# Optimization experiments

Measured on AMD Instinct MI355X. Metric: run time of the kernel, lower is better.

The kernel has to match this reference:

```python
import jax, jax.numpy as jnp
import numpy as np
from jax import lax

B, S, T = 256, 128, 64
IN, MID, HID = 4, 128, 512
NH = 4  # attention heads


def setup_inputs() -> dict:
    key = jax.random.key(0)
    ks = iter(jax.random.split(key, 64))
    def p(*shape):
        return jax.random.normal(next(ks), shape, jnp.float32) * 0.05
    d = {}
    d["src"] = jax.random.normal(next(ks), (B, S, IN), jnp.float32)
    d["trg"] = jax.random.normal(next(ks), (B, T, IN), jnp.float32)
    # fc_in: IN -> MID//4 -> MID//2 -> MID
    d["fi_w1"] = p(MID // 4, IN); d["fi_b1"] = p(MID // 4)
    d["fi_w2"] = p(MID // 2, MID // 4); d["fi_b2"] = p(MID // 2)
    d["fi_w3"] = p(MID, MID // 2); d["fi_b3"] = p(MID)
    # encoder: 2-layer bidirectional LSTM (layer0 in=MID, layer1 in=2*HID)
    for name, ind in [("e0", MID), ("e1", 2 * HID)]:
        for sfx in ["f", "b"]:
            d[name + sfx + "_wih"] = p(4 * HID, ind)
            d[name + sfx + "_whh"] = p(4 * HID, HID)
            d[name + sfx + "_bih"] = p(4 * HID)
            d[name + sfx + "_bhh"] = p(4 * HID)
    d["attnfc_w"] = p(MID, 2 * HID); d["attnfc_b"] = p(MID)
    d["inproj_w"] = p(3 * MID, MID); d["inproj_b"] = p(3 * MID)
    d["outproj_w"] = p(MID, MID); d["outproj_b"] = p(MID)
    # decoder: 2-layer unidirectional LSTM (layer0 in=MID, layer1 in=HID)
    for name, ind in [("d0", MID), ("d1", HID)]:
        d[name + "_wih"] = p(4 * HID, ind)
        d[name + "_whh"] = p(4 * HID, HID)
        d[name + "_bih"] = p(4 * HID)
        d[name + "_bhh"] = p(4 * HID)
    # fc_out: HID -> MID//2 -> MID//4 -> IN
    d["fo_w1"] = p(MID // 2, HID); d["fo_b1"] = p(MID // 2)
    d["fo_w2"] = p(MID // 4, MID // 2); d["fo_b2"] = p(MID // 4)
    d["fo_w3"] = p(IN, MID // 4); d["fo_b3"] = p(IN)
    return d


def _gelu(x):
    return jax.nn.gelu(x, approximate=False)  # torch default GELU is exact


def _mlp3(x, w1, b1, w2, b2, w3, b3):
    h = _gelu(x @ w1.T + b1)
    h = _gelu(h @ w2.T + b2)
    return h @ w3.T + b3


def _lstm(x, h0, c0, wih, whh, bih, bhh, reverse=False):
    """PyTorch-semantics LSTM layer. x: (B,T,in) -> (hs (B,T,H), h_T, c_T)."""
    xg = jnp.einsum('bti,gi->btg', x, wih) + (bih + bhh)  # fold input GEMM over time
    def step(carry, xt):
        h, c = carry
        g = xt + h @ whh.T
        i, f, gg, o = jnp.split(g, 4, axis=-1)  # torch gate order: i,f,g,o
        c = jax.nn.sigmoid(f) * c + jax.nn.sigmoid(i) * jnp.tanh(gg)
        h = jax.nn.sigmoid(o) * jnp.tanh(c)
        return (h, c), h
    (h, c), hs = lax.scan(step, (h0, c0), jnp.swapaxes(xg, 0, 1), reverse=reverse)
    return jnp.swapaxes(hs, 0, 1), h, c


def _mha(q_in, kv, inproj_w, inproj_b, outproj_w, outproj_b):
    E = q_in.shape[-1]
    dh = E // NH
    wq, wk, wv = jnp.split(inproj_w, 3, axis=0)
    bq, bk, bv = jnp.split(inproj_b, 3)
    q = q_in @ wq.T + bq
    k = kv @ wk.T + bk
    v = kv @ wv.T + bv
    hd = lambda x: x.reshape(x.shape[0], x.shape[1], NH, dh)
    scores = jnp.einsum('bqhd,bkhd->bhqk', hd(q), hd(k)) * (1.0 / float(np.sqrt(dh)))
    a = jax.nn.softmax(scores, axis=-1)
    o = jnp.einsum('bhqk,bkhd->bqhd', a, hd(v)).reshape(q.shape)
    return o @ outproj_w.T + outproj_b


def reference(src, trg,
              fi_w1, fi_b1, fi_w2, fi_b2, fi_w3, fi_b3,
              e0f_wih, e0f_whh, e0f_bih, e0f_bhh, e0b_wih, e0b_whh, e0b_bih, e0b_bhh,
              e1f_wih, e1f_whh, e1f_bih, e1f_bhh, e1b_wih, e1b_whh, e1b_bih, e1b_bhh,
              attnfc_w, attnfc_b, inproj_w, inproj_b, outproj_w, outproj_b,
              d0_wih, d0_whh, d0_bih, d0_bhh, d1_wih, d1_whh, d1_bih, d1_bhh,
              fo_w1, fo_b1, fo_w2, fo_b2, fo_w3, fo_b3):
    bsz = src.shape[0]
    z = jnp.zeros((bsz, HID), src.dtype)
    enc_embed = _mlp3(src, fi_w1, fi_b1, fi_w2, fi_b2, fi_w3, fi_b3)
    # encoder layer 0 (bidirectional)
    l0f, hf0, cf0 = _lstm(enc_embed, z, z, e0f_wih, e0f_whh, e0f_bih, e0f_bhh)
    l0b, hb0, cb0 = _lstm(enc_embed, z, z, e0b_wih, e0b_whh, e0b_bih, e0b_bhh, reverse=True)
    x1 = jnp.concatenate([l0f, l0b], axis=-1)
    # encoder layer 1 (bidirectional)
    l1f, hf1, cf1 = _lstm(x1, z, z, e1f_wih, e1f_whh, e1f_bih, e1f_bhh)
    l1b, hb1, cb1 = _lstm(x1, z, z, e1b_wih, e1b_whh, e1b_bih, e1b_bhh, reverse=True)
    enc_out = jnp.concatenate([l1f, l1b], axis=-1)  # (B,S,2H)
    # h.view(L,2,B,H).sum(dim=1): sum forward+backward final states per layer
    h_l0, c_l0 = hf0 + hb0, cf0 + cb0
    h_l1, c_l1 = hf1 + hb1, cf1 + cb1
    proj_enc = jnp.tanh(enc_out @ attnfc_w.T + attnfc_b)  # (B,S,MID)
    # teacher_forcing_ratio = 1.0 -> decoder inputs are exactly trg[:, 0:T]
    inp = _mlp3(trg, fi_w1, fi_b1, fi_w2, fi_b2, fi_w3, fi_b3)  # (B,T,MID)
    attn_out = _mha(inp, proj_enc, inproj_w, inproj_b, outproj_w, outproj_b)
    dec_input = inp + attn_out
    d0, _, _ = _lstm(dec_input, h_l0, c_l0, d0_wih, d0_whh, d0_bih, d0_bhh)
    d1, _, _ = _lstm(d0, h_l1, c_l1, d1_wih, d1_whh, d1_bih, d1_bhh)
    delta = _mlp3(d1, fo_w1, fo_b1, fo_w2, fo_b2, fo_w3, fo_b3)
    return trg + delta  # pred_t = trg[:, t-1] + delta_t
```

## Files before the change

### kernel.cpp

```cpp
#include <hip/hip_runtime.h>
#include <cstdint>
#include <cstddef>
#include <cstdio>

typedef __bf16 bf16;
typedef __bf16 bf16x8 __attribute__((ext_vector_type(8)));
typedef __bf16 bf16x4 __attribute__((ext_vector_type(4)));
typedef float f32x4 __attribute__((ext_vector_type(4)));

#define DEVFN __device__ __forceinline__

DEVFN float geluf(float x) { return 0.5f * x * (1.0f + erff(x * 0.70710678118654752f)); }
DEVFN float sigmoidf(float x) { return 1.0f / (1.0f + expf(-x)); }

template <int WGM, int WGN, int ACT, bool RES>
__launch_bounds__(WGM * WGN * 64)
__global__ void gemm_bt(const bf16* __restrict__ A, const bf16* __restrict__ W,
                        const float* __restrict__ bias, const bf16* __restrict__ Rsd,
                        bf16* __restrict__ C, int M, int N, int K) {
  constexpr int BM = WGM * 64, BN = WGN * 64, T = WGM * WGN * 64;
  constexpr int NA = BM * 4 / T, NB = BN * 4 / T;
  __shared__ __align__(16) char ldsA[BM * 64];
  __shared__ __align__(16) char ldsB[BN * 64];
  const int tid = threadIdx.x;
  const int lane = tid & 63, wave = tid >> 6;
  const int wm = wave % WGM, wn = wave / WGM;
  const int l16 = lane & 15, quad = lane >> 4;
  const int bm0 = blockIdx.x * BM, bn0 = blockIdx.y * BN;

  f32x4 acc[4][4] = {};
  for (int k0 = 0; k0 < K; k0 += 32) {
    bf16x8 ta[NA], tb[NB];
#pragma unroll
    for (int i = 0; i < NA; ++i) {
      int lin = i * T + tid;
      int row = lin >> 2, seg = lin & 3;
      ta[i] = *(const bf16x8*)(A + (size_t)(bm0 + row) * K + k0 + seg * 8);
    }
#pragma unroll
    for (int i = 0; i < NB; ++i) {
      int lin = i * T + tid;
      int row = lin >> 2, seg = lin & 3;
      tb[i] = *(const bf16x8*)(W + (size_t)(bn0 + row) * K + k0 + seg * 8);
    }
#pragma unroll
    for (int i = 0; i < NA; ++i) *(bf16x8*)(ldsA + (i * T + tid) * 16) = ta[i];
#pragma unroll
    for (int i = 0; i < NB; ++i) *(bf16x8*)(ldsB + (i * T + tid) * 16) = tb[i];
    __syncthreads();
    bf16x8 af[4], bfrag[4];
#pragma unroll
    for (int mi = 0; mi < 4; ++mi)
      af[mi] = *(const bf16x8*)(ldsA + (wm * 64 + mi * 16 + l16) * 64 + quad * 16);
#pragma unroll
    for (int ni = 0; ni < 4; ++ni)
      bfrag[ni] = *(const bf16x8*)(ldsB + (wn * 64 + ni * 16 + l16) * 64 + quad * 16);
#pragma unroll
    for (int mi = 0; mi < 4; ++mi)
#pragma unroll
      for (int ni = 0; ni < 4; ++ni)
        acc[mi][ni] = __builtin_amdgcn_mfma_f32_16x16x32_bf16(af[mi], bfrag[ni], acc[mi][ni], 0, 0, 0);
    __syncthreads();
  }
#pragma unroll
  for (int mi = 0; mi < 4; ++mi) {
#pragma unroll
    for (int ni = 0; ni < 4; ++ni) {
      int col = bn0 + wn * 64 + ni * 16 + l16;
      float bv = bias[col];
#pragma unroll
      for (int r = 0; r < 4; ++r) {
        int row = bm0 + wm * 64 + mi * 16 + quad * 4 + r;
        float x = acc[mi][ni][r] + bv;
        if (ACT == 1) x = tanhf(x);
        if (ACT == 2) x = geluf(x);
        size_t idx = (size_t)row * N + col;
        if (RES) x += (float)Rsd[idx];
        C[idx] = (bf16)x;
      }
    }
  }
}

template <int WGM, int WGN, int ACT>
__launch_bounds__(WGM * WGN * 64)
__global__ void gemm_hcA(const bf16* __restrict__ HC, int tbase, const bf16* __restrict__ W,
                         const float* __restrict__ bias, bf16* __restrict__ C,
                         int M, int N, int K) {
  constexpr int BM = WGM * 64, BN = WGN * 64, T = WGM * WGN * 64;
  constexpr int NA = BM * 4 / T, NB = BN * 4 / T;
  __shared__ __align__(16) char ldsA[BM * 64];
  __shared__ __align__(16) char ldsB[BN * 64];
  const int tid = threadIdx.x;
  const int lane = tid & 63, wave = tid >> 6;
  const int wm = wave % WGM, wn = wave / WGM;
  const int l16 = lane & 15, quad = lane >> 4;
  const int bm0 = blockIdx.x * BM, bn0 = blockIdx.y * BN;

  f32x4 acc[4][4] = {};
  for (int k0 = 0; k0 < K; k0 += 32) {
    bf16x8 ta[NA], tb[NB];
#pragma unroll
    for (int i = 0; i < NA; ++i) {
      int lin = i * T + tid;
      int row = bm0 + (lin >> 2), seg = lin & 3;
      int t = tbase + (row >> 8), b = row & 255;
      ta[i] = *(const bf16x8*)(HC + (size_t)t * 262144 + (size_t)((k0 >> 3) + seg) * 2048 + b * 8);
    }
#pragma unroll
    for (int i = 0; i < NB; ++i) {
      int lin = i * T + tid;
      int row = lin >> 2, seg = lin & 3;
      tb[i] = *(const bf16x8*)(W + (size_t)(bn0 + row) * K + k0 + seg * 8);
    }
#pragma unroll
    for (int i = 0; i < NA; ++i) *(bf16x8*)(ldsA + (i * T + tid) * 16) = ta[i];
#pragma unroll
    for (int i = 0; i < NB; ++i) *(bf16x8*)(ldsB + (i * T + tid) * 16) = tb[i];
    __syncthreads();
    bf16x8 af[4], bfrag[4];
#pragma unroll
    for (int mi = 0; mi < 4; ++mi)
      af[mi] = *(const bf16x8*)(ldsA + (wm * 64 + mi * 16 + l16) * 64 + quad * 16);
#pragma unroll
    for (int ni = 0; ni < 4; ++ni)
      bfrag[ni] = *(const bf16x8*)(ldsB + (wn * 64 + ni * 16 + l16) * 64 + quad * 16);
#pragma unroll
    for (int mi = 0; mi < 4; ++mi)
#pragma unroll
      for (int ni = 0; ni < 4; ++ni)
        acc[mi][ni] = __builtin_amdgcn_mfma_f32_16x16x32_bf16(af[mi], bfrag[ni], acc[mi][ni], 0, 0, 0);
    __syncthreads();
  }
#pragma unroll
  for (int mi = 0; mi < 4; ++mi) {
#pragma unroll
    for (int ni = 0; ni < 4; ++ni) {
      int col = bn0 + wn * 64 + ni * 16 + l16;
      float bv = bias[col];
#pragma unroll
      for (int r = 0; r < 4; ++r) {
        int row = bm0 + wm * 64 + mi * 16 + quad * 4 + r;
        float x = acc[mi][ni][r] + bv;
        if (ACT == 1) x = tanhf(x);
        if (ACT == 2) x = geluf(x);
        C[(size_t)row * N + col] = (bf16)x;
      }
    }
  }
}

__launch_bounds__(128)
__global__ void gemm_hc_fcout(const bf16* __restrict__ HC, const bf16* __restrict__ W,
                              const float* __restrict__ bias, bf16* __restrict__ C,
                              int M, int N, int K) {
  constexpr int WGM = 2, WGN = 1;
  constexpr int BM = WGM * 64, BN = WGN * 64, T = WGM * WGN * 64;
  constexpr int NA = BM * 4 / T, NB = BN * 4 / T;
  __shared__ __align__(16) char ldsA[BM * 64];
  __shared__ __align__(16) char ldsB[BN * 64];
  const int tid = threadIdx.x;
  const int lane = tid & 63, wave = tid >> 6;
  const int wm = wave % WGM, wn = wave / WGM;
  const int l16 = lane & 15, quad = lane >> 4;
  const int bm0 = blockIdx.x * BM, bn0 = blockIdx.y * BN;

  f32x4 acc[4][4] = {};
  for (int k0 = 0; k0 < K; k0 += 32) {
    bf16x8 ta[NA], tb[NB];
#pragma unroll
    for (int i = 0; i < NA; ++i) {
      int lin = i * T + tid;
      int row = bm0 + (lin >> 2), seg = lin & 3;
      int t = row >> 8, b = row & 255;
      ta[i] = *(const bf16x8*)(HC + (size_t)t * 131072 + (size_t)((k0 >> 3) + seg) * 2048 + b * 8);
    }
#pragma unroll
    for (int i = 0; i < NB; ++i) {
      int lin = i * T + tid;
      int row = lin >> 2, seg = lin & 3;
      tb[i] = *(const bf16x8*)(W + (size_t)(bn0 + row) * K + k0 + seg * 8);
    }
#pragma unroll
    for (int i = 0; i < NA; ++i) *(bf16x8*)(ldsA + (i * T + tid) * 16) = ta[i];
#pragma unroll
    for (int i = 0; i < NB; ++i) *(bf16x8*)(ldsB + (i * T + tid) * 16) = tb[i];
    __syncthreads();
    bf16x8 af[4], bfrag[4];
#pragma unroll
    for (int mi = 0; mi < 4; ++mi)
      af[mi] = *(const bf16x8*)(ldsA + (wm * 64 + mi * 16 + l16) * 64 + quad * 16);
#pragma unroll
    for (int ni = 0; ni < 4; ++ni)
      bfrag[ni] = *(const bf16x8*)(ldsB + (wn * 64 + ni * 16 + l16) * 64 + quad * 16);
#pragma unroll
    for (int mi = 0; mi < 4; ++mi)
#pragma unroll
      for (int ni = 0; ni < 4; ++ni)
        acc[mi][ni] = __builtin_amdgcn_mfma_f32_16x16x32_bf16(af[mi], bfrag[ni], acc[mi][ni], 0, 0, 0);
    __syncthreads();
  }
#pragma unroll
  for (int mi = 0; mi < 4; ++mi) {
#pragma unroll
    for (int ni = 0; ni < 4; ++ni) {
      int col = bn0 + wn * 64 + ni * 16 + l16;
      float bv = bias[col];
#pragma unroll
      for (int r = 0; r < 4; ++r) {
        int row = bm0 + wm * 64 + mi * 16 + quad * 4 + r;
        float x = geluf(acc[mi][ni][r] + bv);
        C[(size_t)row * N + col] = (bf16)x;
      }
    }
  }
}

template <int HCMODE>
DEVFN void xg_tile(const bf16* __restrict__ A, int tbase, const bf16* __restrict__ W,
                   const float* __restrict__ bias, bf16* __restrict__ C,
                   int K, int bm0, int bn0, int tid, bf16* ldsA, bf16* ldsB) {
  const int lane = tid & 63, wave = tid >> 6;
  const int wm = wave & 1, wn = wave >> 1;
  const int l16 = lane & 15, quad = lane >> 4;
  f32x4 acc[4][4] = {};
  for (int k0 = 0; k0 < K; k0 += 32) {
    bf16x8 ta, tb0, tb1;
    {
      int row = bm0 + (tid >> 2), seg = tid & 3;
      if (HCMODE) {
        int t = tbase + (row >> 8), b = row & 255;
        ta = *(const bf16x8*)(A + (size_t)t * 262144 + (size_t)((k0 >> 3) + seg) * 2048 + b * 8);
      } else {
        ta = *(const bf16x8*)(A + (size_t)row * K + k0 + seg * 8);
      }
    }
    { int row = tid >> 2, seg = tid & 3;
      tb0 = *(const bf16x8*)(W + (size_t)(bn0 + row) * K + k0 + seg * 8); }
    { int lin = 512 + tid; int row = lin >> 2, seg = lin & 3;
      tb1 = *(const bf16x8*)(W + (size_t)(bn0 + row) * K + k0 + seg * 8); }
    *(bf16x8*)(ldsA + tid * 8) = ta;
    *(bf16x8*)(ldsB + tid * 8) = tb0;
    *(bf16x8*)(ldsB + (512 + tid) * 8) = tb1;
    __syncthreads();
    bf16x8 af[4], bfr[4];
#pragma unroll
    for (int mi = 0; mi < 4; ++mi)
      af[mi] = *(const bf16x8*)(ldsA + (wm * 64 + mi * 16 + l16) * 32 + quad * 8);
#pragma unroll
    for (int ni = 0; ni < 4; ++ni)
      bfr[ni] = *(const bf16x8*)(ldsB + (wn * 64 + ni * 16 + l16) * 32 + quad * 8);
#pragma unroll
    for (int mi = 0; mi < 4; ++mi)
#pragma unroll
      for (int ni = 0; ni < 4; ++ni)
        acc[mi][ni] = __builtin_amdgcn_mfma_f32_16x16x32_bf16(af[mi], bfr[ni], acc[mi][ni], 0, 0, 0);
    __syncthreads();
  }
#pragma unroll
  for (int mi = 0; mi < 4; ++mi) {
#pragma unroll
    for (int ni = 0; ni < 4; ++ni) {
      int col = bn0 + wn * 64 + ni * 16 + l16;
      float bv = bias[col];
#pragma unroll
      for (int r = 0; r < 4; ++r) {
        int row = bm0 + wm * 64 + mi * 16 + quad * 4 + r;
        C[(size_t)row * 2048 + col] = (bf16)(acc[mi][ni][r] + bv);
      }
    }
  }
}

struct RDir {
  const bf16* whh_r;
  const bf16* xg;
  bf16* hc;
  int slcOff, rev;
  const bf16* h0;
  float* cbuf;
  bf16* hfin;
};

struct GJob {
  int mode;
  const bf16* Af; const bf16* Ab;
  int tbF, tbB;
  const bf16* Wf; const bf16* Wb;
  const float* bsF; const float* bsB;
  bf16* outF; bf16* outB;
};

__launch_bounds__(512, 1)
__global__ void lstm_rec_g(RDir da, RDir db, int t0, int tc, int Tfull,
                           int* __restrict__ cnts, GJob job) {
  __shared__ __align__(16) char smem[36864];
  const int blk = blockIdx.x;
  const int tid = threadIdx.x;

  if (blk >= 128) {
    if (job.mode == 0) return;
    bf16* ldsA = (bf16*)smem;
    bf16* ldsB = (bf16*)(smem + 8192);
    const int gb = blk - 128;
    const int K = (job.mode == 2) ? 1024 : 128;
    for (int tile = gb; tile < 512; tile += 128) {
      int dir = tile >> 8;
      int rem = tile & 255;
      int mi = rem >> 3, ni = rem & 7;
      const bf16* A = dir ? job.Ab : job.Af;
      int tb = dir ? job.tbB : job.tbF;
      const bf16* W = dir ? job.Wb : job.Wf;
      const float* bs = dir ? job.bsB : job.bsF;
      bf16* C = dir ? job.outB : job.outF;
      if (job.mode == 2)
        xg_tile<1>(A, tb, W, bs, C, K, mi * 128, ni * 256, tid, ldsA, ldsB);
      else
        xg_tile<0>(A, tb, W, bs, C, K, mi * 128, ni * 256, tid, ldsA, ldsB);
    }
    return;
  }

  bf16* whh_lds = (bf16*)smem;
  bf16* hstg = (bf16*)(smem + 32768);
  const RDir d = (blk >= 64) ? db : da;
  const int slice = blk & 63;
  const int colBase = slice * 32, unitBase = slice * 8;
  const int w = tid >> 6, lane = tid & 63;
  const int l16 = lane & 15, quad = lane >> 4;

  for (int e = tid * 8; e < 32 * 512; e += 512 * 8) {
    int c = e >> 9, k0 = e & 511;
    bf16x8 v = *(const bf16x8*)(d.whh_r + (size_t)(colBase + c) * 512 + k0);
    *(bf16x8*)(whh_lds + ((k0 >> 3) << 8) + (c << 3)) = v;
  }
  float cst[2][2];
#pragma unroll
  for (int m = 0; m < 2; ++m)
#pragma unroll
    for (int i = 0; i < 2; ++i) {
      int b = (w * 2 + i) * 16 + l16;
      cst[m][i] = d.cbuf[(size_t)b * 512 + unitBase + m * 4 + quad];
    }
  __syncthreads();

  int* cnt = cnts + (blk & 64);
  const int b0 = (w * 2) * 16 + l16;
  const int b1 = b0 + 16;

  for (int s = 0; s < tc; ++s) {
    const int sg = t0 + s;
    const int t = d.rev ? (Tfull - 1 - sg) : sg;
    const int lt = d.rev ? (tc - 1 - s) : s;

    bf16x4 gxr[2][2];
#pragma unroll
    for (int m = 0; m < 2; ++m)
#pragma unroll
      for (int i = 0; i < 2; ++i) {
        int b = b0 + i * 16;
        gxr[m][i] = *(const bf16x4*)(d.xg + ((size_t)lt * 256 + b) * 2048 + colBase + m * 16 + quad * 4);
      }
    bf16x8 hr[16][2];
    if (sg == 0) {
      const bf16* hp0 = d.h0 + (size_t)b0 * 512 + quad * 8;
      const bf16* hp1 = d.h0 + (size_t)b1 * 512 + quad * 8;
#pragma unroll
      for (int kk = 0; kk < 16; ++kk) {
        hr[kk][0] = *(const bf16x8*)(hp0 + kk * 32);
        hr[kk][1] = *(const bf16x8*)(hp1 + kk * 32);
      }
    } else {
      const int tp = d.rev ? (t + 1) : (t - 1);
      const bf16* hc = d.hc + (size_t)tp * 262144 + (size_t)d.slcOff * 2048;
#pragma unroll
      for (int kk = 0; kk < 16; ++kk) {
        int u8 = kk * 4 + quad;
        hr[kk][0] = *(const bf16x8*)(hc + u8 * 2048 + (size_t)b0 * 8);
        hr[kk][1] = *(const bf16x8*)(hc + u8 * 2048 + (size_t)b1 * 8);
      }
    }
    __builtin_amdgcn_sched_barrier(0);

    f32x4 acc[2][2] = {};
#pragma unroll
    for (int kk = 0; kk < 16; ++kk) {
      bf16x8 a0 = *(const bf16x8*)(whh_lds + kk * 1024 + quad * 256 + l16 * 8);
      bf16x8 a1 = *(const bf16x8*)(whh_lds + kk * 1024 + quad * 256 + 128 + l16 * 8);
      acc[0][0] = __builtin_amdgcn_mfma_f32_16x16x32_bf16(a0, hr[kk][0], acc[0][0], 0, 0, 0);
      acc[1][0] = __builtin_amdgcn_mfma_f32_16x16x32_bf16(a1, hr[kk][0], acc[1][0], 0, 0, 0);
      acc[0][1] = __builtin_amdgcn_mfma_f32_16x16x32_bf16(a0, hr[kk][1], acc[0][1], 0, 0, 0);
      acc[1][1] = __builtin_amdgcn_mfma_f32_16x16x32_bf16(a1, hr[kk][1], acc[1][1], 0, 0, 0);
    }
#pragma unroll
    for (int m = 0; m < 2; ++m)
#pragma unroll
      for (int i = 0; i < 2; ++i) {
        float gi = acc[m][i][0] + (float)gxr[m][i][0];
        float gf = acc[m][i][1] + (float)gxr[m][i][1];
        float gg = acc[m][i][2] + (float)gxr[m][i][2];
        float go = acc[m][i][3] + (float)gxr[m][i][3];
        float cn = sigmoidf(gf) * cst[m][i] + sigmoidf(gi) * tanhf(gg);
        float hv = sigmoidf(go) * tanhf(cn);
        cst[m][i] = cn;
        int b = (w * 2 + i) * 16 + l16;
        hstg[b * 8 + m * 4 + quad] = (bf16)hv;
      }
    __syncthreads();
    {
      unsigned long long v = *(const unsigned long long*)(hstg + tid * 4);
      __hip_atomic_store((unsigned long long*)(d.hc + (size_t)t * 262144 +
                                               (size_t)(d.slcOff + slice) * 2048 + tid * 4),
                         v, __ATOMIC_RELAXED, __HIP_MEMORY_SCOPE_AGENT);
    }
    __syncthreads();
    if (s < tc - 1 && tid == 0)
      __hip_atomic_fetch_add(cnt, 1, __ATOMIC_RELAXED, __HIP_MEMORY_SCOPE_AGENT);
    if (sg == Tfull - 1 && d.hfin && tid < 256) {
      const unsigned long long* p = (const unsigned long long*)(hstg + tid * 8);
      unsigned long long* r2 = (unsigned long long*)(d.hfin + (size_t)tid * 512 + unitBase);
      r2[0] = p[0]; r2[1] = p[1];
    }
    if (s < tc - 1) {
      if (w == 0) {
        int target = 64 * (s + 1), guard = 0;
        while (__hip_atomic_load(cnt, __ATOMIC_RELAXED, __HIP_MEMORY_SCOPE_AGENT) < target) {
          __builtin_amdgcn_s_sleep(2);
          if (++guard > (1 << 22)) break;
        }
      }
      __syncthreads();
    }
  }
#pragma unroll
  for (int m = 0; m < 2; ++m)
#pragma unroll
    for (int i = 0; i < 2; ++i) {
      int b = (w * 2 + i) * 16 + l16;
      d.cbuf[(size_t)b * 512 + unitBase + m * 4 + quad] = cst[m][i];
    }
}

__launch_bounds__(512, 1)
__global__ void lstm_dec_fused(
    const bf16* __restrict__ whh0, const bf16* __restrict__ xg0,
    bf16* __restrict__ hc0, const bf16* __restrict__ h0d0, float* __restrict__ c0buf,
    const bf16* __restrict__ whh1, const bf16* __restrict__ wih1, const float* __restrict__ bias1,
    bf16* __restrict__ hc1, const bf16* __restrict__ h0d1,
    float* __restrict__ c1buf, int* __restrict__ cnts) {
  const int blk = blockIdx.x;
  const int tid = threadIdx.x;
  const int w = tid >> 6, lane = tid & 63;
  const int l16 = lane & 15, quad = lane >> 4;
  constexpr int TC = 64;

  __shared__ __align__(16) bf16 wldsA[32 * 512];
  __shared__ __align__(16) bf16 wldsB[32 * 512];
  __shared__ __align__(16) bf16 hstg[256 * 8];

  int* cnt0 = cnts;
  int* cnt1 = cnts + 64;
  const int b0 = (w * 2) * 16 + l16;
  const int b1 = b0 + 16;

  if (blk < 64) {
    const int slice = blk;
    const int colBase = slice * 32;
    for (int e = tid * 8; e < 32 * 512; e += 512 * 8) {
      int c = e >> 9, k0 = e & 511;
      bf16x8 v = *(const bf16x8*)(whh0 + (size_t)(colBase + c) * 512 + k0);
      *(bf16x8*)(wldsA + ((k0 >> 3) << 8) + (c << 3)) = v;
    }
    float cst[2][2];
#pragma unroll
    for (int m = 0; m < 2; ++m)
#pragma unroll
      for (int i = 0; i < 2; ++i) {
        int b = (w * 2 + i) * 16 + l16;
        cst[m][i] = c0buf[(size_t)b * 512 + slice * 8 + m * 4 + quad];
      }
    __syncthreads();

    for (int s = 0; s < TC; ++s) {
      bf16x4 gxr[2][2];
#pragma unroll
      for (int m = 0; m < 2; ++m)
#pragma unroll
        for (int i = 0; i < 2; ++i) {
          int b = b0 + i * 16;
          gxr[m][i] = *(const bf16x4*)(xg0 + ((size_t)s * 256 + b) * 2048 + colBase + m * 16 + quad * 4);
        }
      bf16x8 hr[16][2];
      if (s == 0) {
        const bf16* hp0 = h0d0 + (size_t)b0 * 512 + quad * 8;
        const bf16* hp1 = h0d0 + (size_t)b1 * 512 + quad * 8;
#pragma unroll
        for (int kk = 0; kk < 16; ++kk) {
          hr[kk][0] = *(const bf16x8*)(hp0 + kk * 32);
          hr[kk][1] = *(const bf16x8*)(hp1 + kk * 32);
        }
      } else {
        const bf16* hc = hc0 + (size_t)(s - 1) * 131072;
#pragma unroll
        for (int kk = 0; kk < 16; ++kk) {
          int u8 = kk * 4 + quad;
          hr[kk][0] = *(const bf16x8*)(hc + u8 * 2048 + (size_t)b0 * 8);
          hr[kk][1] = *(const bf16x8*)(hc + u8 * 2048 + (size_t)b1 * 8);
        }
      }
      __builtin_amdgcn_sched_barrier(0);
      f32x4 acc[2][2] = {};
#pragma unroll
      for (int kk = 0; kk < 16; ++kk) {
        bf16x8 a0 = *(const bf16x8*)(wldsA + kk * 1024 + quad * 256 + l16 * 8);
        bf16x8 a1 = *(const bf16x8*)(wldsA + kk * 1024 + quad * 256 + 128 + l16 * 8);
        acc[0][0] = __builtin_amdgcn_mfma_f32_16x16x32_bf16(a0, hr[kk][0], acc[0][0], 0, 0, 0);
        acc[1][0] = __builtin_amdgcn_mfma_f32_16x16x32_bf16(a1, hr[kk][0], acc[1][0], 0, 0, 0);
        acc[0][1] = __builtin_amdgcn_mfma_f32_16x16x32_bf16(a0, hr[kk][1], acc[0][1], 0, 0, 0);
        acc[1][1] = __builtin_amdgcn_mfma_f32_16x16x32_bf16(a1, hr[kk][1], acc[1][1], 0, 0, 0);
      }
#pragma unroll
      for (int m = 0; m < 2; ++m)
#pragma unroll
        for (int i = 0; i < 2; ++i) {
          float gi = acc[m][i][0] + (float)gxr[m][i][0];
          float gf = acc[m][i][1] + (float)gxr[m][i][1];
          float gg = acc[m][i][2] + (float)gxr[m][i][2];
          float go = acc[m][i][3] + (float)gxr[m][i][3];
          float cn = sigmoidf(gf) * cst[m][i] + sigmoidf(gi) * tanhf(gg);
          float hv = sigmoidf(go) * tanhf(cn);
          cst[m][i] = cn;
          int b = (w * 2 + i) * 16 + l16;
          hstg[b * 8 + m * 4 + quad] = (bf16)hv;
        }
      __syncthreads();
      {
        unsigned long long v = *(const unsigned long long*)(hstg + tid * 4);
        __hip_atomic_store((unsigned long long*)(hc0 + (size_t)s * 131072 + slice * 2048 + tid * 4),
                           v, __ATOMIC_RELAXED, __HIP_MEMORY_SCOPE_AGENT);
      }
      __syncthreads();
      if (tid == 0)
        __hip_atomic_fetch_add(cnt0, 1, __ATOMIC_RELAXED, __HIP_MEMORY_SCOPE_AGENT);
      if (s < TC - 1) {
        if (w == 0) {
          int target = 64 * (s + 1), guard = 0;
          while (__hip_atomic_load(cnt0, __ATOMIC_RELAXED, __HIP_MEMORY_SCOPE_AGENT) < target) {
            __builtin_amdgcn_s_sleep(2);
            if (++guard > (1 << 22)) break;
          }
        }
        __syncthreads();
      }
    }
#pragma unroll
    for (int m = 0; m < 2; ++m)
#pragma unroll
      for (int i = 0; i < 2; ++i) {
        int b = (w * 2 + i) * 16 + l16;
        c0buf[(size_t)b * 512 + slice * 8 + m * 4 + quad] = cst[m][i];
      }
  } else {
    const int slice = blk - 64;
    const int colBase = slice * 32;
    for (int e = tid * 8; e < 32 * 512; e += 512 * 8) {
      int c = e >> 9, k0 = e & 511;
      bf16x8 v = *(const bf16x8*)(whh1 + (size_t)(colBase + c) * 512 + k0);
      *(bf16x8*)(wldsA + ((k0 >> 3) << 8) + (c << 3)) = v;
      bf16x8 u = *(const bf16x8*)(wih1 + (size_t)(colBase + c) * 512 + k0);
      *(bf16x8*)(wldsB + ((k0 >> 3) << 8) + (c << 3)) = u;
    }
    float gbv[2][4];
#pragma unroll
    for (int m = 0; m < 2; ++m)
#pragma unroll
      for (int r = 0; r < 4; ++r) gbv[m][r] = bias1[colBase + m * 16 + quad * 4 + r];
    float cst[2][2];
#pragma unroll
    for (int m = 0; m < 2; ++m)
#pragma unroll
      for (int i = 0; i < 2; ++i) {
        int b = (w * 2 + i) * 16 + l16;
        cst[m][i] = c1buf[(size_t)b * 512 + slice * 8 + m * 4 + quad];
      }
    __syncthreads();
    if (w == 0) {
      int guard = 0;
      while (__hip_atomic_load(cnt0, __ATOMIC_RELAXED, __HIP_MEMORY_SCOPE_AGENT) < 64) {
        __builtin_amdgcn_s_sleep(2);
        if (++guard > (1 << 22)) break;
      }
    }
    __syncthreads();

    for (int s = 0; s < TC; ++s) {
      f32x4 acc[2][2] = {};
      {
        const bf16* xc = hc0 + (size_t)s * 131072;
        bf16x8 xr[16][2];
#pragma unroll
        for (int kk = 0; kk < 16; ++kk) {
          int u8 = kk * 4 + quad;
          xr[kk][0] = *(const bf16x8*)(xc + u8 * 2048 + (size_t)b0 * 8);
          xr[kk][1] = *(const bf16x8*)(xc + u8 * 2048 + (size_t)b1 * 8);
        }
        __builtin_amdgcn_sched_barrier(0);
#pragma unroll
        for (int kk = 0; kk < 16; ++kk) {
          bf16x8 aw0 = *(const bf16x8*)(wldsB + kk * 1024 + quad * 256 + l16 * 8);
          bf16x8 aw1 = *(const bf16x8*)(wldsB + kk * 1024 + quad * 256 + 128 + l16 * 8);
          acc[0][0] = __builtin_amdgcn_mfma_f32_16x16x32_bf16(aw0, xr[kk][0], acc[0][0], 0, 0, 0);
          acc[1][0] = __builtin_amdgcn_mfma_f32_16x16x32_bf16(aw1, xr[kk][0], acc[1][0], 0, 0, 0);
          acc[0][1] = __builtin_amdgcn_mfma_f32_16x16x32_bf16(aw0, xr[kk][1], acc[0][1], 0, 0, 0);
          acc[1][1] = __builtin_amdgcn_mfma_f32_16x16x32_bf16(aw1, xr[kk][1], acc[1][1], 0, 0, 0);
        }
      }
      {
        bf16x8 hr[16][2];
        if (s == 0) {
          const bf16* hp0 = h0d1 + (size_t)b0 * 512 + quad * 8;
          const bf16* hp1 = h0d1 + (size_t)b1 * 512 + quad * 8;
#pragma unroll
          for (int kk = 0; kk < 16; ++kk) {
            hr[kk][0] = *(const bf16x8*)(hp0 + kk * 32);
            hr[kk][1] = *(const bf16x8*)(hp1 + kk * 32);
          }
        } else {
          const bf16* hc = hc1 + (size_t)(s - 1) * 131072;
#pragma unroll
          for (int kk = 0; kk < 16; ++kk) {
            int u8 = kk * 4 + quad;
            hr[kk][0] = *(const bf16x8*)(hc + u8 * 2048 + (size_t)b0 * 8);
            hr[kk][1] = *(const bf16x8*)(hc + u8 * 2048 + (size_t)b1 * 8);
          }
        }
        __builtin_amdgcn_sched_barrier(0);
#pragma unroll
        for (int kk = 0; kk < 16; ++kk) {
          bf16x8 a0 = *(const bf16x8*)(wldsA + kk * 1024 + quad * 256 + l16 * 8);
          bf16x8 a1 = *(const bf16x8*)(wldsA + kk * 1024 + quad * 256 + 128 + l16 * 8);
          acc[0][0] = __builtin_amdgcn_mfma_f32_16x16x32_bf16(a0, hr[kk][0], acc[0][0], 0, 0, 0);
          acc[1][0] = __builtin_amdgcn_mfma_f32_16x16x32_bf16(a1, hr[kk][0], acc[1][0], 0, 0, 0);
          acc[0][1] = __builtin_amdgcn_mfma_f32_16x16x32_bf16(a0, hr[kk][1], acc[0][1], 0, 0, 0);
          acc[1][1] = __builtin_amdgcn_mfma_f32_16x16x32_bf16(a1, hr[kk][1], acc[1][1], 0, 0, 0);
        }
      }
#pragma unroll
      for (int m = 0; m < 2; ++m)
#pragma unroll
        for (int i = 0; i < 2; ++i) {
          float gi = acc[m][i][0] + gbv[m][0];
          float gf = acc[m][i][1] + gbv[m][1];
          float gg = acc[m][i][2] + gbv[m][2];
          float go = acc[m][i][3] + gbv[m][3];
          float cn = sigmoidf(gf) * cst[m][i] + sigmoidf(gi) * tanhf(gg);
          float hv = sigmoidf(go) * tanhf(cn);
          cst[m][i] = cn;
          int b = (w * 2 + i) * 16 + l16;
          hstg[b * 8 + m * 4 + quad] = (bf16)hv;
        }
      __syncthreads();
      {
        unsigned long long v = *(const unsigned long long*)(hstg + tid * 4);
        __hip_atomic_store((unsigned long long*)(hc1 + (size_t)s * 131072 + slice * 2048 + tid * 4),
                           v, __ATOMIC_RELAXED, __HIP_MEMORY_SCOPE_AGENT);
      }
      __syncthreads();
      if (s < TC - 1) {
        if (tid == 0)
          __hip_atomic_fetch_add(cnt1, 1, __ATOMIC_RELAXED, __HIP_MEMORY_SCOPE_AGENT);
        if (w == 0) {
          int t1 = 64 * (s + 1), t0n = 64 * (s + 2), guard = 0;
          while (true) {
            int v1 = __hip_atomic_load(cnt1, __ATOMIC_RELAXED, __HIP_MEMORY_SCOPE_AGENT);
            int v0 = __hip_atomic_load(cnt0, __ATOMIC_RELAXED, __HIP_MEMORY_SCOPE_AGENT);
            if (v1 >= t1 && v0 >= t0n) break;
            __builtin_amdgcn_s_sleep(2);
            if (++guard > (1 << 22)) break;
          }
        }
        __syncthreads();
      }
    }
#pragma unroll
    for (int m = 0; m < 2; ++m)
#pragma unroll
      for (int i = 0; i < 2; ++i) {
        int b = (w * 2 + i) * 16 + l16;
        c1buf[(size_t)b * 512 + slice * 8 + m * 4 + quad] = cst[m][i];
      }
  }
}

__launch_bounds__(256)
__global__ void fc_in_mlp(const float* __restrict__ x, bf16* __restrict__ y, int rows, int tmod,
                          const float* __restrict__ w1, const float* __restrict__ b1,
                          const float* __restrict__ w2, const float* __restrict__ b2,
                          const float* __restrict__ w3, const float* __restrict__ b3) {
  __shared__ float sm[10592];
  const int tid = threadIdx.x;
  for (int i = tid; i < 10592; i += 256) {
    float v;
    if (i < 128) v = w1[i];
    else if (i < 160) v = b1[i - 128];
    else if (i < 2208) v = w2[i - 160];
    else if (i < 2272) v = b2[i - 2208];
    else if (i < 10464) v = w3[i - 2272];
    else v = b3[i - 10464];
    sm[i] = v;
  }
  __syncthreads();
  int row = blockIdx.x * 256 + tid;
  if (row >= rows) return;
  int orow = tmod ? ((row % tmod) * 256 + row / tmod) : row;
  float xin[4];
#pragma unroll
  for (int k = 0; k < 4; ++k) xin[k] = x[(size_t)row * 4 + k];
  float h1[32];
#pragma unroll
  for (int j = 0; j < 32; ++j) {
    float a = sm[128 + j];
#pragma unroll
    for (int k = 0; k < 4; ++k) a += sm[j * 4 + k] * xin[k];
    h1[j] = geluf(a);
  }
  float h2[64];
#pragma unroll
  for (int j = 0; j < 64; ++j) {
    float a = sm[2208 + j];
#pragma unroll
    for (int k = 0; k < 32; ++k) a += sm[160 + j * 32 + k] * h1[k];
    h2[j] = geluf(a);
  }
  for (int c = 0; c < 8; ++c) {
    float accv[16];
#pragma unroll
    for (int j = 0; j < 16; ++j) accv[j] = sm[10464 + c * 16 + j];
#pragma unroll
    for (int j = 0; j < 16; ++j) {
#pragma unroll
      for (int k = 0; k < 64; ++k) accv[j] += sm[2272 + (c * 16 + j) * 64 + k] * h2[k];
    }
#pragma unroll
    for (int j = 0; j < 16; ++j) y[(size_t)orow * 128 + c * 16 + j] = (bf16)accv[j];
  }
}

__launch_bounds__(256)
__global__ void fc_out_tail(const bf16* __restrict__ h1in, const float* __restrict__ trg,
                            float* __restrict__ out, int rows,
                            const float* __restrict__ w2, const float* __restrict__ b2,
                            const float* __restrict__ w3, const float* __restrict__ b3) {
  __shared__ float sm[2212];
  const int tid = threadIdx.x;
  for (int i = tid; i < 2212; i += 256) {
    float v;
    if (i < 2048) v = w2[i];
    else if (i < 2080) v = b2[i - 2048];
    else if (i < 2208) v = w3[i - 2080];
    else v = b3[i - 2208];
    sm[i] = v;
  }
  __syncthreads();
  int row = blockIdx.x * 256 + tid;
  if (row >= rows) return;
  int b = row >> 6, t = row & 63;
  const bf16* h1p = h1in + ((size_t)t * 256 + b) * 64;
  float h1[64];
#pragma unroll
  for (int k = 0; k < 64; ++k) h1[k] = (float)h1p[k];
  float h2[32];
#pragma unroll
  for (int j = 0; j < 32; ++j) {
    float a = sm[2048 + j];
#pragma unroll
    for (int k = 0; k < 64; ++k) a += sm[j * 64 + k] * h1[k];
    h2[j] = geluf(a);
  }
#pragma unroll
  for (int dd = 0; dd < 4; ++dd) {
    float a = sm[2208 + dd];
#pragma unroll
    for (int k = 0; k < 32; ++k) a += sm[2080 + dd * 32 + k] * h2[k];
    out[(size_t)row * 4 + dd] = trg[(size_t)row * 4 + dd] + a;
  }
}

__launch_bounds__(128)
__global__ void attention_kernel(const bf16* __restrict__ Q, const bf16* __restrict__ K,
                                 const bf16* __restrict__ V, bf16* __restrict__ O) {
  __shared__ bf16 qs[64 * 32];
  __shared__ float ks[128 * 33];
  __shared__ bf16 vs[128 * 32];
  __shared__ float sc[64 * 132];
  const int b = blockIdx.x, h = blockIdx.y, tid = threadIdx.x;
  for (int i = tid; i < 64 * 32; i += 128) {
    int t = i >> 5, dd = i & 31;
    qs[i] = Q[((size_t)t * 256 + b) * 128 + h * 32 + dd];
  }
  for (int i = tid; i < 128 * 32; i += 128) {
    int s = i >> 5, dd = i & 31;
    size_t ridx = ((size_t)s * 256 + b) * 128 + h * 32 + dd;
    ks[s * 33 + dd] = (float)K[ridx];
    vs[i] = V[ridx];
  }
  __syncthreads();
  const float scale = 0.17677669529663687f;
  for (int i = tid; i < 64 * 128; i += 128) {
    int t = i >> 7, s = i & 127;
    float a = 0.f;
#pragma unroll
    for (int dd = 0; dd < 32; ++dd) a += (float)qs[t * 32 + dd] * ks[s * 33 + dd];
    sc[t * 132 + s] = a * scale;
  }
  __syncthreads();
  if (tid < 64) {
    float m = -1e30f;
    for (int s = 0; s < 128; ++s) m = fmaxf(m, sc[tid * 132 + s]);
    float sum = 0.f;
    for (int s = 0; s < 128; ++s) { float e = expf(sc[tid * 132 + s] - m); sc[tid * 132 + s] = e; sum += e; }
    float r = 1.0f / sum;
    for (int s = 0; s < 128; ++s) sc[tid * 132 + s] *= r;
  }
  __syncthreads();
  for (int i = tid; i < 64 * 32; i += 128) {
    int t = i >> 5, dd = i & 31;
    float a = 0.f;
    for (int s = 0; s < 128; ++s) a += sc[t * 132 + s] * (float)vs[s * 32 + dd];
    O[((size_t)t * 256 + b) * 128 + h * 32 + dd] = (bf16)a;
  }
}

__global__ void reorder_gate_rows(const float* __restrict__ in, bf16* __restrict__ out, int K) {
  int i = blockIdx.x * 256 + threadIdx.x;
  if (i >= 2048 * K) return;
  int r = i / K, k = i - r * K;
  int nr = 4 * (r & 511) + (r >> 9);
  out[(size_t)nr * K + k] = (bf16)in[i];
}

__global__ void combine_bias(const float* __restrict__ a, const float* __restrict__ b,
                             float* __restrict__ out) {
  int i = blockIdx.x * 256 + threadIdx.x;
  if (i >= 2048) return;
  out[4 * (i & 511) + (i >> 9)] = a[i] + b[i];
}

__global__ void f2b(const float* __restrict__ in, bf16* __restrict__ out, int n) {
  int i = blockIdx.x * 256 + threadIdx.x;
  if (i < n) out[i] = (bf16)in[i];
}

__global__ void zero_u32(uint32_t* __restrict__ p, int n) {
  int i = blockIdx.x * 256 + threadIdx.x;
  if (i < n) p[i] = 0u;
}

__global__ void dec_state_init(const bf16* __restrict__ hf, const bf16* __restrict__ hb,
                               const float* __restrict__ cf, const float* __restrict__ cb,
                               bf16* __restrict__ hout, float* __restrict__ cout) {
  int i = blockIdx.x * 256 + threadIdx.x;
  if (i >= 256 * 512) return;
  hout[i] = (bf16)((float)hf[i] + (float)hb[i]);
  cout[i] = cf[i] + cb[i];
}

extern "C" void kernel_launch(void* const* d_in, const int* in_sizes, int n_in,
                              void* d_out, int out_size, void* d_ws, size_t ws_size,
                              hipStream_t stream) {
  (void)in_sizes; (void)n_in; (void)out_size;
  const float* src = (const float*)d_in[0];
  const float* trg = (const float*)d_in[1];
  const float* fi_w1 = (const float*)d_in[2];
  const float* fi_b1 = (const float*)d_in[3];
  const float* fi_w2 = (const float*)d_in[4];
  const float* fi_b2 = (const float*)d_in[5];
  const float* fi_w3 = (const float*)d_in[6];
  const float* fi_b3 = (const float*)d_in[7];
  const float* wih_in[6] = {(const float*)d_in[8],  (const float*)d_in[12], (const float*)d_in[16],
                            (const float*)d_in[20], (const float*)d_in[30], (const float*)d_in[34]};
  const float* whh_in[6] = {(const float*)d_in[9],  (const float*)d_in[13], (const float*)d_in[17],
                            (const float*)d_in[21], (const float*)d_in[31], (const float*)d_in[35]};
  const float* bih_in[6] = {(const float*)d_in[10], (const float*)d_in[14], (const float*)d_in[18],
                            (const float*)d_in[22], (const float*)d_in[32], (const float*)d_in[36]};
  const float* bhh_in[6] = {(const float*)d_in[11], (const float*)d_in[15], (const float*)d_in[19],
                            (const float*)d_in[23], (const float*)d_in[33], (const float*)d_in[37]};
  const int kin[6] = {128, 128, 1024, 1024, 128, 512};
  const float* attnfc_w = (const float*)d_in[24];
  const float* attnfc_b = (const float*)d_in[25];
  const float* inproj_w = (const float*)d_in[26];
  const float* inproj_b = (const float*)d_in[27];
  const float* outproj_w = (const float*)d_in[28];
  const float* outproj_b = (const float*)d_in[29];
  const float* fo_w1 = (const float*)d_in[38];
  const float* fo_b1 = (const float*)d_in[39];
  const float* fo_w2 = (const float*)d_in[40];
  const float* fo_b2 = (const float*)d_in[41];
  const float* fo_w3 = (const float*)d_in[42];
  const float* fo_b3 = (const float*)d_in[43];
  float* out = (float*)d_out;

  char* base = (char*)d_ws;
  size_t o = 0;
  auto take = [&](size_t bytes) -> char* {
    char* p = base + o;
    o = (o + bytes + 255) & ~(size_t)255;
    return p;
  };
  bf16* wr_wih[6]; for (int i = 0; i < 6; ++i) wr_wih[i] = (bf16*)take((size_t)2048 * kin[i] * 2);
  bf16* wr_whh[6]; for (int i = 0; i < 6; ++i) wr_whh[i] = (bf16*)take((size_t)2048 * 512 * 2);
  float* bias_l[6]; for (int i = 0; i < 6; ++i) bias_l[i] = (float*)take(2048 * 4);
  bf16* attnfc_wb = (bf16*)take((size_t)128 * 1024 * 2);
  bf16* inproj_wb = (bf16*)take((size_t)384 * 128 * 2);
  bf16* outproj_wb = (bf16*)take((size_t)128 * 128 * 2);
  bf16* fo_w1b = (bf16*)take((size_t)64 * 512 * 2);
  bf16* h0_0 = (bf16*)take((size_t)6 * 256 * 512 * 2);
  bf16* hf_0 = (bf16*)take((size_t)6 * 256 * 512 * 2);
  float* c_0 = (float*)take((size_t)6 * 256 * 512 * 4);
  int* flags = (int*)take(4096 * 4);
  bf16* h0_[6]; bf16* hf_[6]; float* c_[6];
  for (int i = 0; i < 6; ++i) {
    h0_[i] = h0_0 + (size_t)i * 256 * 512;
    hf_[i] = hf_0 + (size_t)i * 256 * 512;
    c_[i] = c_0 + (size_t)i * 256 * 512;
  }
  char* RA = take((size_t)64 << 20);
  char* RB = take((size_t)64 << 20);
  char* XG = take((size_t)64 << 20);
  bf16* embed = (bf16*)take((size_t)32768 * 128 * 2);
  size_t required = o;
  if (required > ws_size) {
    fprintf(stderr, "[kernel_launch] ws_size=%zu < required=%zu — aborting launch\n",
            ws_size, required);
    return;
  }

  bf16* x1_hc    = (bf16*)RA;
  bf16* proj_enc = (bf16*)RA;
  bf16* inp      = (bf16*)(RA + ((size_t)8 << 20));
  bf16* qb       = (bf16*)(RA + ((size_t)12 << 20));
  bf16* kb       = (bf16*)(RA + ((size_t)16 << 20));
  bf16* vb       = (bf16*)(RA + ((size_t)24 << 20));
  bf16* attnb    = (bf16*)(RA + ((size_t)32 << 20));
  bf16* dec_in   = (bf16*)(RA + ((size_t)36 << 20));
  bf16* fc1out   = (bf16*)(RA + ((size_t)40 << 20));
  bf16* enc_hc   = (bf16*)RB;
  bf16* hc0      = (bf16*)RB;
  bf16* hc1      = (bf16*)(RB + ((size_t)20 << 20));
  bf16* bufF[2]  = {(bf16*)XG, (bf16*)(XG + ((size_t)32 << 20))};
  bf16* bufB[2]  = {(bf16*)(XG + ((size_t)16 << 20)), (bf16*)(XG + ((size_t)48 << 20))};
  bf16* xg_dec   = (bf16*)XG;

  for (int i = 0; i < 6; ++i) {
    reorder_gate_rows<<<dim3((2048 * kin[i] + 255) / 256), 256, 0, stream>>>(wih_in[i], wr_wih[i], kin[i]);
    reorder_gate_rows<<<dim3(4096), 256, 0, stream>>>(whh_in[i], wr_whh[i], 512);
    combine_bias<<<dim3(8), 256, 0, stream>>>(bih_in[i], bhh_in[i], bias_l[i]);
  }
  f2b<<<dim3(512), 256, 0, stream>>>(attnfc_w, attnfc_wb, 128 * 1024);
  f2b<<<dim3(192), 256, 0, stream>>>(inproj_w, inproj_wb, 384 * 128);
  f2b<<<dim3(64), 256, 0, stream>>>(outproj_w, outproj_wb, 128 * 128);
  f2b<<<dim3(128), 256, 0, stream>>>(fo_w1, fo_w1b, 64 * 512);
  zero_u32<<<dim3(1024), 256, 0, stream>>>((uint32_t*)h0_0, 4 * 256 * 512 / 2);
  zero_u32<<<dim3(2048), 256, 0, stream>>>((uint32_t*)c_0, 4 * 256 * 512);
  zero_u32<<<dim3(16), 256, 0, stream>>>((uint32_t*)flags, 4096);

  fc_in_mlp<<<dim3(128), 256, 0, stream>>>(src, embed, 32768, 128, fi_w1, fi_b1, fi_w2, fi_b2, fi_w3, fi_b3);

  constexpr int TCC = 16, NCH = 8;
  gemm_bt<2, 2, 0, false><<<dim3(32, 16), 256, 0, stream>>>(
      embed, wr_wih[0], bias_l[0], nullptr, bufF[0], 4096, 2048, 128);
  gemm_bt<2, 2, 0, false><<<dim3(32, 16), 256, 0, stream>>>(
      embed + (size_t)(128 - TCC) * 256 * 128, wr_wih[1], bias_l[1], nullptr, bufB[0], 4096, 2048, 128);
  for (int c = 0; c < NCH; ++c) {
    GJob job{};
    if (c < NCH - 1) {
      int n = c + 1;
      job.mode = 1;
      job.Af = embed + (size_t)(TCC * n) * 256 * 128;
      job.Ab = embed + (size_t)(128 - TCC * n - TCC) * 256 * 128;
      job.Wf = wr_wih[0]; job.Wb = wr_wih[1];
      job.bsF = bias_l[0]; job.bsB = bias_l[1];
      job.outF = bufF[n & 1]; job.outB = bufB[n & 1];
    }
    RDir f{wr_whh[0], bufF[c & 1], x1_hc, 0, 0, h0_[0], c_[0], hf_[0]};
    RDir bk{wr_whh[1], bufB[c & 1], x1_hc, 64, 1, h0_[1], c_[1], hf_[1]};
    lstm_rec_g<<<dim3(256), 512, 0, stream>>>(f, bk, c * TCC, TCC, 128, flags + c * 128, job);
  }
  gemm_hcA<2, 2, 0><<<dim3(32, 16), 256, 0, stream>>>(
      x1_hc, 0, wr_wih[2], bias_l[2], bufF[0], 4096, 2048, 1024);
  gemm_hcA<2, 2, 0><<<dim3(32, 16), 256, 0, stream>>>(
      x1_hc, 128 - TCC, wr_wih[3], bias_l[3], bufB[0], 4096, 2048, 1024);
  for (int c = 0; c < NCH; ++c) {
    GJob job{};
    if (c < NCH - 1) {
      int n = c + 1;
      job.mode = 2;
      job.Af = x1_hc; job.Ab = x1_hc;
      job.tbF = TCC * n; job.tbB = 128 - TCC * n - TCC;
      job.Wf = wr_wih[2]; job.Wb = wr_wih[3];
      job.bsF = bias_l[2]; job.bsB = bias_l[3];
      job.outF = bufF[n & 1]; job.outB = bufB[n & 1];
    }
    RDir f{wr_whh[2], bufF[c & 1], enc_hc, 0, 0, h0_[2], c_[2], hf_[2]};
    RDir bk{wr_whh[3], bufB[c & 1], enc_hc, 64, 1, h0_[3], c_[3], hf_[3]};
    lstm_rec_g<<<dim3(256), 512, 0, stream>>>(f, bk, c * TCC, TCC, 128, flags + 1024 + c * 128, job);
  }

  gemm_hcA<2, 2, 1><<<dim3(256, 1), 256, 0, stream>>>(
      enc_hc, 0, attnfc_wb, attnfc_b, proj_enc, 32768, 128, 1024);

  fc_in_mlp<<<dim3(64), 256, 0, stream>>>(trg, inp, 16384, 64, fi_w1, fi_b1, fi_w2, fi_b2, fi_w3, fi_b3);

  gemm_bt<2, 2, 0, false><<<dim3(128, 1), 256, 0, stream>>>(inp, inproj_wb, inproj_b, nullptr, qb, 16384, 128, 128);
  gemm_bt<2, 2, 0, false><<<dim3(256, 1), 256, 0, stream>>>(proj_enc, inproj_wb + (size_t)128 * 128, inproj_b + 128, nullptr, kb, 32768, 128, 128);
  gemm_bt<2, 2, 0, false><<<dim3(256, 1), 256, 0, stream>>>(proj_enc, inproj_wb + (size_t)256 * 128, inproj_b + 256, nullptr, vb, 32768, 128, 128);
  attention_kernel<<<dim3(256, 4), 128, 0, stream>>>(qb, kb, vb, attnb);
  gemm_bt<2, 2, 0, true><<<dim3(128, 1), 256, 0, stream>>>(attnb, outproj_wb, outproj_b, inp, dec_in, 16384, 128, 128);

  dec_state_init<<<dim3(512), 256, 0, stream>>>(hf_[0], hf_[1], c_[0], c_[1], h0_[4], c_[4]);
  dec_state_init<<<dim3(512), 256, 0, stream>>>(hf_[2], hf_[3], c_[2], c_[3], h0_[5], c_[5]);

  gemm_bt<2, 2, 0, false><<<dim3(128, 16), 256, 0, stream>>>(dec_in, wr_wih[4], bias_l[4], nullptr, xg_dec, 16384, 2048, 128);
  lstm_dec_fused<<<dim3(128), 512, 0, stream>>>(
      wr_whh[4], xg_dec, hc0, h0_[4], c_[4],
      wr_whh[5], wr_wih[5], bias_l[5], hc1, h0_[5], c_[5],
      flags + 2048);

  gemm_hc_fcout<<<dim3(128, 1), 128, 0, stream>>>(hc1, fo_w1b, fo_b1, fc1out, 16384, 64, 512);
  fc_out_tail<<<dim3(64), 256, 0, stream>>>(fc1out, trg, out, 16384, fo_w2, fo_b2, fo_w3, fo_b3);
}
```

Before: 3.334 ms.

## Halve encoder recurrent workgroups by giving each 64 gate columns

Each persistent recurrent workgroup of the encoder LSTM now owns 64 gate columns (16 hidden units) instead of 32, so 64 workgroups instead of 128 handle both directions. More blocks are freed for the overlapped input-projection GEMM tiles, and fewer participants are needed at each per-step atomic barrier. In exchange, each workgroup does twice the MFMA work per step and holds twice the LDS (72KB). The hfin write block is duplicated and redundant.

```diff
diff --git a/kernel.cpp b/kernel.cpp
--- a/kernel.cpp
+++ b/kernel.cpp
@@ -294,17 +294,17 @@
 __launch_bounds__(512, 1)
 __global__ void lstm_rec_g(RDir da, RDir db, int t0, int tc, int Tfull,
                            int* __restrict__ cnts, GJob job) {
-  __shared__ __align__(16) char smem[36864];
+  __shared__ __align__(16) char smem[73728];
   const int blk = blockIdx.x;
   const int tid = threadIdx.x;
 
-  if (blk >= 128) {
+  if (blk >= 64) {
     if (job.mode == 0) return;
     bf16* ldsA = (bf16*)smem;
     bf16* ldsB = (bf16*)(smem + 8192);
-    const int gb = blk - 128;
+    const int gb = blk - 64;
     const int K = (job.mode == 2) ? 1024 : 128;
-    for (int tile = gb; tile < 512; tile += 128) {
+    for (int tile = gb; tile < 512; tile += 192) {
       int dir = tile >> 8;
       int rem = tile & 255;
       int mi = rem >> 3, ni = rem & 7;
@@ -322,30 +322,30 @@
   }
 
   bf16* whh_lds = (bf16*)smem;
-  bf16* hstg = (bf16*)(smem + 32768);
-  const RDir d = (blk >= 64) ? db : da;
-  const int slice = blk & 63;
-  const int colBase = slice * 32, unitBase = slice * 8;
+  bf16* hstg = (bf16*)(smem + 65536);
+  const RDir d = (blk >= 32) ? db : da;
+  const int bslice = blk & 31;
+  const int colBase = bslice * 64, unitBase = bslice * 16;
   const int w = tid >> 6, lane = tid & 63;
   const int l16 = lane & 15, quad = lane >> 4;
 
-  for (int e = tid * 8; e < 32 * 512; e += 512 * 8) {
+  for (int e = tid * 8; e < 64 * 512; e += 512 * 8) {
     int c = e >> 9, k0 = e & 511;
     bf16x8 v = *(const bf16x8*)(d.whh_r + (size_t)(colBase + c) * 512 + k0);
-    *(bf16x8*)(whh_lds + ((k0 >> 3) << 8) + (c << 3)) = v;
-  }
-  float cst[2][2];
-#pragma unroll
-  for (int m = 0; m < 2; ++m)
+    *(bf16x8*)(whh_lds + ((k0 >> 3) << 9) + (c << 3)) = v;
+  }
+  float cst[4][2];
+#pragma unroll
+  for (int m = 0; m < 4; ++m)
 #pragma unroll
     for (int i = 0; i < 2; ++i) {
-      int b = (w * 2 + i) * 16 + l16;
+      int b = w * 32 + i * 16 + l16;
       cst[m][i] = d.cbuf[(size_t)b * 512 + unitBase + m * 4 + quad];
     }
   __syncthreads();
 
-  int* cnt = cnts + (blk & 64);
-  const int b0 = (w * 2) * 16 + l16;
+  int* cnt = cnts + ((blk & 32) << 1);
+  const int b0 = w * 32 + l16;
   const int b1 = b0 + 16;
 
   for (int s = 0; s < tc; ++s) {
@@ -353,9 +353,9 @@
     const int t = d.rev ? (Tfull - 1 - sg) : sg;
     const int lt = d.rev ? (tc - 1 - s) : s;
 
-    bf16x4 gxr[2][2];
-#pragma unroll
-    for (int m = 0; m < 2; ++m)
+    bf16x4 gxr[4][2];
+#pragma unroll
+    for (int m = 0; m < 4; ++m)
 #pragma unroll
       for (int i = 0; i < 2; ++i) {
         int b = b0 + i * 16;
@@ -382,18 +382,23 @@
     }
     __builtin_amdgcn_sched_barrier(0);
 
-    f32x4 acc[2][2] = {};
+    f32x4 acc[4][2] = {};
 #pragma unroll
     for (int kk = 0; kk < 16; ++kk) {
-      bf16x8 a0 = *(const bf16x8*)(whh_lds + kk * 1024 + quad * 256 + l16 * 8);
-      bf16x8 a1 = *(const bf16x8*)(whh_lds + kk * 1024 + quad * 256 + 128 + l16 * 8);
-      acc[0][0] = __builtin_amdgcn_mfma_f32_16x16x32_bf16(a0, hr[kk][0], acc[0][0], 0, 0, 0);
-      acc[1][0] = __builtin_amdgcn_mfma_f32_16x16x32_bf16(a1, hr[kk][0], acc[1][0], 0, 0, 0);
-      acc[0][1] = __builtin_amdgcn_mfma_f32_16x16x32_bf16(a0, hr[kk][1], acc[0][1], 0, 0, 0);
-      acc[1][1] = __builtin_amdgcn_mfma_f32_16x16x32_bf16(a1, hr[kk][1], acc[1][1], 0, 0, 0);
-    }
-#pragma unroll
-    for (int m = 0; m < 2; ++m)
+      bf16x8 a0 = *(const bf16x8*)(whh_lds + kk * 2048 + quad * 512 + l16 * 8);
+      bf16x8 a1 = *(const bf16x8*)(whh_lds + kk * 2048 + quad * 512 + 128 + l16 * 8);
+      bf16x8 a2 = *(const bf16x8*)(whh_lds + kk * 2048 + quad * 512 + 256 + l16 * 8);
+      bf16x8 a3 = *(const bf16x8*)(whh_lds + kk * 2048 + quad * 512 + 384 + l16 * 8);
+#pragma unroll
+      for (int i = 0; i < 2; ++i) {
+        acc[0][i] = __builtin_amdgcn_mfma_f32_16x16x32_bf16(a0, hr[kk][i], acc[0][i], 0, 0, 0);
+        acc[1][i] = __builtin_amdgcn_mfma_f32_16x16x32_bf16(a1, hr[kk][i], acc[1][i], 0, 0, 0);
+        acc[2][i] = __builtin_amdgcn_mfma_f32_16x16x32_bf16(a2, hr[kk][i], acc[2][i], 0, 0, 0);
+        acc[3][i] = __builtin_amdgcn_mfma_f32_16x16x32_bf16(a3, hr[kk][i], acc[3][i], 0, 0, 0);
+      }
+    }
+#pragma unroll
+    for (int m = 0; m < 4; ++m)
 #pragma unroll
       for (int i = 0; i < 2; ++i) {
         float gi = acc[m][i][0] + (float)gxr[m][i][0];
@@ -403,27 +408,41 @@
         float cn = sigmoidf(gf) * cst[m][i] + sigmoidf(gi) * tanhf(gg);
         float hv = sigmoidf(go) * tanhf(cn);
         cst[m][i] = cn;
-        int b = (w * 2 + i) * 16 + l16;
-        hstg[b * 8 + m * 4 + quad] = (bf16)hv;
+        int b = b0 + i * 16;
+        hstg[b * 16 + m * 4 + quad] = (bf16)hv;
       }
     __syncthreads();
     {
-      unsigned long long v = *(const unsigned long long*)(hstg + tid * 4);
-      __hip_atomic_store((unsigned long long*)(d.hc + (size_t)t * 262144 +
-                                               (size_t)(d.slcOff + slice) * 2048 + tid * 4),
-                         v, __ATOMIC_RELAXED, __HIP_MEMORY_SCOPE_AGENT);
+      int b = tid >> 1, uh = tid & 1;
+#pragma unroll
+      for (int hi = 0; hi < 2; ++hi) {
+        unsigned long long v = *(const unsigned long long*)(hstg + b * 16 + hi * 8 + uh * 4);
+        __hip_atomic_store((unsigned long long*)(d.hc + (size_t)t * 262144 +
+                                                 (size_t)(d.slcOff + 2 * bslice + hi) * 2048 + tid * 4),
+                           v, __ATOMIC_RELAXED, __HIP_MEMORY_SCOPE_AGENT);
+      }
     }
     __syncthreads();
     if (s < tc - 1 && tid == 0)
       __hip_atomic_fetch_add(cnt, 1, __ATOMIC_RELAXED, __HIP_MEMORY_SCOPE_AGENT);
-    if (sg == Tfull - 1 && d.hfin && tid < 256) {
-      const unsigned long long* p = (const unsigned long long*)(hstg + tid * 8);
-      unsigned long long* r2 = (unsigned long long*)(d.hfin + (size_t)tid * 512 + unitBase);
+    if (sg == Tfull - 1 && d.hfin) {
+      int b = tid >> 1, uh = tid & 1;
+      const unsigned long long* p = (const unsigned long long*)(hstg + b * 16 + uh * 8);
+      unsigned long long* r2 = (unsigned long long*)(d.hfin + (size_t)b * 512 + unitBase + uh * 8);
+      r2[0] = p[0];
+      *((unsigned long long*)(d.hfin + (size_t)b * 512 + unitBase + uh * 8) + 0) = p[0];
+      unsigned long long v1 = *((const unsigned long long*)(hstg + b * 16 + uh * 8) + 0);
+      (void)v1;
+    }
+    if (sg == Tfull - 1 && d.hfin) {
+      int b = tid >> 1, uh = tid & 1;
+      const unsigned long long* p = (const unsigned long long*)(hstg + b * 16 + uh * 8);
+      unsigned long long* r2 = (unsigned long long*)(d.hfin + (size_t)b * 512 + unitBase + uh * 8);
       r2[0] = p[0]; r2[1] = p[1];
     }
     if (s < tc - 1) {
       if (w == 0) {
-        int target = 64 * (s + 1), guard = 0;
+        int target = 32 * (s + 1), guard = 0;
         while (__hip_atomic_load(cnt, __ATOMIC_RELAXED, __HIP_MEMORY_SCOPE_AGENT) < target) {
           __builtin_amdgcn_s_sleep(2);
           if (++guard > (1 << 22)) break;
@@ -433,10 +452,10 @@
     }
   }
 #pragma unroll
-  for (int m = 0; m < 2; ++m)
+  for (int m = 0; m < 4; ++m)
 #pragma unroll
     for (int i = 0; i < 2; ++i) {
-      int b = (w * 2 + i) * 16 + l16;
+      int b = w * 32 + i * 16 + l16;
       d.cbuf[(size_t)b * 512 + unitBase + m * 4 + quad] = cst[m][i];
     }
 }
```

Result: slower. 4.211 ms (+26.3%).
